# Optimization experiments

Hardware: AMD Instinct MI355X
Metric: run time of the kernel (lower is better)

Reference implementation:

```python
import jax, jax.numpy as jnp
import numpy as np

EPS = 1e-12
N_POS, N_NEG, N_NEUT, N_ASSAS = 9, 8, 7, 1
VOCAB_K = 512  # vocab_size: number of search results
NEUT_W, NEG_W, ASSAS_W = 1.0, 0.0, -10.0


def _normalize(x):
    # F.normalize(p=2, dim=-1)
    return x / jnp.maximum(jnp.linalg.norm(x, axis=-1, keepdims=True), EPS)


def _pool(embs):
    # mean over dim 1, then L2-normalize
    return _normalize(jnp.mean(embs, axis=1))


def setup_inputs() -> dict:
    key = jax.random.key(0)
    ks = jax.random.split(key, 10)
    B = 64
    inp = {
        "pos_embs": jax.random.normal(ks[0], (B, N_POS, 768), jnp.float32),
        "neg_embs": jax.random.normal(ks[1], (B, N_NEG, 768), jnp.float32),
        "neut_embs": jax.random.normal(ks[2], (B, N_NEUT, 768), jnp.float32),
        "assas_emb": jax.random.normal(ks[3], (B, 768), jnp.float32),
        "vocab_table": jax.random.normal(ks[4], (100000, 768), jnp.float32),
        "W1": jax.random.normal(ks[5], (3072, 2304), jnp.float32) * 0.02,
        "b1": jnp.zeros((2304,), jnp.float32),
        "W2": jax.random.normal(ks[6], (2304, 1700), jnp.float32) * 0.02,
        "b2": jnp.zeros((1700,), jnp.float32),
        "W3": jax.random.normal(ks[7], (1700, 1000), jnp.float32) * 0.02,
        "b3": jnp.zeros((1000,), jnp.float32),
        "W4": jax.random.normal(ks[8], (1000, 768), jnp.float32) * 0.02,
        "b4": jnp.zeros((768,), jnp.float32),
    }
    return inp


def _forward(pos_embs, neg_embs, neut_embs, assas_emb, vocab_table,
             W1, b1, W2, b2, W3, b3, W4, b4):
    # --- combined input: cat(neg_pool, assas, neut_pool, pos_pool) -> [B, 3072]
    concatenated = jnp.concatenate(
        [_pool(neg_embs), assas_emb, _pool(neut_embs), _pool(pos_embs)], axis=1)

    # --- fc MLP with tanh activations (none after last layer)
    h = jnp.tanh(concatenated @ W1 + b1)
    h = jnp.tanh(h @ W2 + b2)
    h = jnp.tanh(h @ W3 + b3)
    model_out = _normalize(h @ W4 + b4)  # [B, 768]

    # --- vocab.search: top-VOCAB_K cosine similarity against vocab table
    vocab_norm = _normalize(vocab_table)            # [N, 768]
    sims = model_out @ vocab_norm.T                  # [B, N]
    _, top_idx = jax.lax.top_k(sims, VOCAB_K)        # [B, V]
    word_embeddings = vocab_table[top_idx]           # [B, V, 768]

    # --- cosine scores against each board group (normalize then dot)
    wn = _normalize(word_embeddings)                 # [B, V, 768]
    pos_s = jnp.einsum('bvd,bpd->bvp', wn, _normalize(pos_embs))    # [B,V,9]
    neg_s = jnp.einsum('bvd,bpd->bvp', wn, _normalize(neg_embs))    # [B,V,8]
    neut_s = jnp.einsum('bvd,bpd->bvp', wn, _normalize(neut_embs))  # [B,V,7]
    assas_s = jnp.einsum('bvd,bd->bv', wn, _normalize(assas_emb))[..., None]  # [B,V,1]

    # --- primary reward: # of positive words ranked before first non-positive
    combined = jnp.concatenate([pos_s, neg_s, neut_s, assas_s], axis=2)  # [B,V,25]
    order = jnp.argsort(-combined, axis=2)           # descending sort indices
    reward_vec = jnp.concatenate(
        [jnp.zeros((N_POS,), jnp.float32),
         jnp.ones((N_NEG + N_NEUT + N_ASSAS,), jnp.float32)])
    rewards = reward_vec[order]                      # [B,V,25]
    primary = jnp.argmax(rewards, axis=2).astype(jnp.float32)  # [B,V]

    # --- secondary reward: weight of the highest-scoring non-positive word
    combined2 = combined[:, :, N_POS:]               # [B,V,16]
    reward_vec2 = jnp.concatenate(
        [jnp.full((N_NEG,), NEG_W, jnp.float32),
         jnp.full((N_NEUT,), NEUT_W, jnp.float32),
         jnp.full((N_ASSAS,), ASSAS_W, jnp.float32)])
    secondary = reward_vec2[jnp.argmax(combined2, axis=2)]      # [B,V]

    tot_reward = primary + secondary                 # [B,V]

    # --- topk(V//2) max / min selection, gather, mean-pool, normalize
    k = VOCAB_K // 2
    _, idx_max = jax.lax.top_k(tot_reward, k)
    _, idx_min = jax.lax.top_k(-tot_reward, k)
    emb_max = jnp.take_along_axis(word_embeddings, idx_max[:, :, None], axis=1)
    emb_min = jnp.take_along_axis(word_embeddings, idx_min[:, :, None], axis=1)
    max_pooled = _pool(emb_max)
    min_pooled = _pool(emb_min)
    search_embedding = emb_max[:, 0]                 # highest-scoring embedding

    return model_out, search_embedding, max_pooled, min_pooled


def reference(pos_embs, neg_embs, neut_embs, assas_emb, vocab_table,
              W1, b1, W2, b2, W3, b3, W4, b4):
    return _forward(pos_embs, neg_embs, neut_embs, assas_emb, vocab_table,
                    W1, b1, W2, b2, W3, b3, W4, b4)
```

## Files before the change

### kernel.cpp

```cpp
#include <hip/hip_runtime.h>
#include <hip/hip_bf16.h>
#include <stdint.h>

#define B_    64
#define D_    768
#define NVOC  100000
#define VK    512
#define KH    256
#define NPART 4
#define PLEN  25000

typedef __attribute__((ext_vector_type(8))) short short8v;
typedef __attribute__((ext_vector_type(4))) float f32x4;

__device__ __forceinline__ float b2f_raw(unsigned short u) {
    return __uint_as_float(((unsigned int)u) << 16);
}
__device__ __forceinline__ float ldin(const void* p, size_t i, int isbf) {
    return isbf ? b2f_raw(((const unsigned short*)p)[i]) : ((const float*)p)[i];
}
__device__ __forceinline__ float4 ldin4(const void* p, size_t i, int isbf) {
    if (isbf) {
        ushort4 r = *(const ushort4*)((const unsigned short*)p + i);
        return make_float4(b2f_raw(r.x), b2f_raw(r.y), b2f_raw(r.z), b2f_raw(r.w));
    }
    return *(const float4*)((const float*)p + i);
}
__device__ __forceinline__ unsigned short f2bf(float x) {
    uint32_t u = __float_as_uint(x);
    uint32_t r = (u + 0x7FFFu + ((u >> 16) & 1u)) >> 16;
    return (unsigned short)r;
}
__device__ __forceinline__ uint32_t fmono(float x) {
    uint32_t u = __float_as_uint(x);
    return u ^ (uint32_t)((((int32_t)u) >> 31) | 0x80000000u);
}

__device__ __forceinline__ float block_reduce_sum_256(float v, float* red) {
    int tid = threadIdx.x;
    red[tid] = v; __syncthreads();
    #pragma unroll
    for (int s = 128; s > 0; s >>= 1) {
        if (tid < s) red[tid] += red[tid + s];
        __syncthreads();
    }
    float r = red[0]; __syncthreads();
    return r;
}

__global__ void detect_kernel(const void* vocab, int* flag) {
    if (threadIdx.x == 0 && blockIdx.x == 0) {
        const float* vf = (const float*)vocab;
        int sane = 0;
        for (int i = 0; i < 256; i++) {
            float a = fabsf(vf[i]);
            if (a > 1e-4f && a < 64.0f) sane++;
        }
        *flag = (sane >= 200) ? 0 : 1;
    }
}

__global__ __launch_bounds__(256) void prep_kernel(
    const void* __restrict__ pos, const void* __restrict__ neg,
    const void* __restrict__ neut, const void* __restrict__ assas,
    float* __restrict__ concat, float* __restrict__ invemb,
    const int* __restrict__ dflag) {
    __shared__ float red[256];
    int isbf = *dflag;
    int b = blockIdx.x, tid = threadIdx.x;
    int d = tid * 3;
    const void* srcs[3] = {pos, neg, neut};
    const int cnts[3]  = {9, 8, 7};
    const int ieoff[3] = {0, 9, 17};
    const int coff[3]  = {2304, 0, 1536};
    for (int g = 0; g < 3; g++) {
        float m0 = 0.f, m1 = 0.f, m2 = 0.f;
        int cnt = cnts[g];
        for (int m = 0; m < cnt; m++) {
            size_t base = ((size_t)b * cnt + m) * D_ + d;
            float x0 = ldin(srcs[g], base + 0, isbf);
            float x1 = ldin(srcs[g], base + 1, isbf);
            float x2 = ldin(srcs[g], base + 2, isbf);
            float S = block_reduce_sum_256(x0 * x0 + x1 * x1 + x2 * x2, red);
            if (tid == 0)
                invemb[b * 25 + ieoff[g] + m] = 1.0f / fmaxf(sqrtf(S), 1e-12f);
            m0 += x0; m1 += x1; m2 += x2;
        }
        float invc = 1.0f / (float)cnt;
        m0 *= invc; m1 *= invc; m2 *= invc;
        float S = block_reduce_sum_256(m0 * m0 + m1 * m1 + m2 * m2, red);
        float inv = 1.0f / fmaxf(sqrtf(S), 1e-12f);
        float* o = concat + (size_t)b * 3072 + coff[g] + d;
        o[0] = m0 * inv; o[1] = m1 * inv; o[2] = m2 * inv;
    }
    size_t abase = (size_t)b * D_ + d;
    float x0 = ldin(assas, abase + 0, isbf);
    float x1 = ldin(assas, abase + 1, isbf);
    float x2 = ldin(assas, abase + 2, isbf);
    float* oc = concat + (size_t)b * 3072 + 768 + d;
    oc[0] = x0; oc[1] = x1; oc[2] = x2;
    float S = block_reduce_sum_256(x0 * x0 + x1 * x1 + x2 * x2, red);
    if (tid == 0) invemb[b * 25 + 24] = 1.0f / fmaxf(sqrtf(S), 1e-12f);
}

__global__ __launch_bounds__(256) void gemm_partial_kernel(
    const float* __restrict__ X, const void* __restrict__ W,
    float* __restrict__ P, int K, int N, int CH, const int* __restrict__ dflag) {
    __shared__ float xs[64][68];
    __shared__ float wt[64][68];
    int isbf = *dflag;
    int tid = threadIdx.x;
    int n0 = blockIdx.x * 64;
    int kstart = blockIdx.y * CH;
    int kend = min(K, kstart + CH);
    int tx = tid & 15, ty = tid >> 4;
    float acc[4][4] = {{0.f}};
    for (int k0 = kstart; k0 < kend; k0 += 64) {
        #pragma unroll
        for (int q = 0; q < 4; q++) {
            int e4 = tid + q * 256;
            int m = e4 >> 4, kk = (e4 & 15) * 4;
            float4 v = make_float4(0.f, 0.f, 0.f, 0.f);
            if (k0 + kk < kend) v = *(const float4*)(X + (size_t)m * K + k0 + kk);
            xs[kk + 0][m] = v.x; xs[kk + 1][m] = v.y;
            xs[kk + 2][m] = v.z; xs[kk + 3][m] = v.w;
        }
        #pragma unroll
        for (int q = 0; q < 4; q++) {
            int e4 = tid + q * 256;
            int kk = e4 >> 4, c = (e4 & 15) * 4;
            float4 v = make_float4(0.f, 0.f, 0.f, 0.f);
            if (k0 + kk < kend && n0 + c < N)
                v = ldin4(W, (size_t)(k0 + kk) * N + n0 + c, isbf);
            wt[kk][c + 0] = v.x; wt[kk][c + 1] = v.y;
            wt[kk][c + 2] = v.z; wt[kk][c + 3] = v.w;
        }
        __syncthreads();
        #pragma unroll 16
        for (int kk = 0; kk < 64; kk++) {
            float4 a = *(const float4*)&xs[kk][ty * 4];
            float4 w = *(const float4*)&wt[kk][tx * 4];
            acc[0][0] += a.x * w.x; acc[0][1] += a.x * w.y; acc[0][2] += a.x * w.z; acc[0][3] += a.x * w.w;
            acc[1][0] += a.y * w.x; acc[1][1] += a.y * w.y; acc[1][2] += a.y * w.z; acc[1][3] += a.y * w.w;
            acc[2][0] += a.z * w.x; acc[2][1] += a.z * w.y; acc[2][2] += a.z * w.z; acc[2][3] += a.z * w.w;
            acc[3][0] += a.w * w.x; acc[3][1] += a.w * w.y; acc[3][2] += a.w * w.z; acc[3][3] += a.w * w.w;
        }
        __syncthreads();
    }
    size_t base = (size_t)blockIdx.y * 64 * N;
    int n = n0 + tx * 4;
    if (n < N) {
        #pragma unroll
        for (int i = 0; i < 4; i++) {
            float4 o = make_float4(acc[i][0], acc[i][1], acc[i][2], acc[i][3]);
            *(float4*)(P + base + (size_t)(ty * 4 + i) * N + n) = o;
        }
    }
}

__global__ __launch_bounds__(256) void reduce_act_kernel(
    const float* __restrict__ P, const void* __restrict__ bias,
    float* __restrict__ Y, int N, int KS, int act, const int* __restrict__ dflag) {
    int isbf = *dflag;
    int idx = blockIdx.x * 256 + threadIdx.x;
    if (idx >= 64 * N) return;
    int n = idx % N;
    float s = 0.f;
    for (int ks = 0; ks < KS; ks++) s += P[(size_t)ks * 64 * N + idx];
    s += ldin(bias, n, isbf);
    if (act) s = tanhf(s);
    Y[idx] = s;
}

__global__ __launch_bounds__(256) void norm_mo_kernel(
    float* __restrict__ mo, float* __restrict__ out, float* __restrict__ moTp,
    unsigned short* __restrict__ moA) {
    __shared__ float red[256];
    int b = blockIdx.x, tid = threadIdx.x, d = tid * 3;
    float* r_ = mo + (size_t)b * D_ + d;
    float x0 = r_[0], x1 = r_[1], x2 = r_[2];
    float S = block_reduce_sum_256(x0 * x0 + x1 * x1 + x2 * x2, red);
    float inv = 1.0f / fmaxf(sqrtf(S), 1e-12f);
    x0 *= inv; x1 *= inv; x2 *= inv;
    r_[0] = x0; r_[1] = x1; r_[2] = x2;
    float* o = out + (size_t)b * D_ + d;
    o[0] = x0; o[1] = x1; o[2] = x2;
    if (moTp) {
        moTp[(size_t)(d + 0) * 64 + b] = x0;
        moTp[(size_t)(d + 1) * 64 + b] = x1;
        moTp[(size_t)(d + 2) * 64 + b] = x2;
    }
    if (moA) {
        float xv[3] = {x0, x1, x2};
        int w = b >> 4;
        #pragma unroll
        for (int c = 0; c < 3; c++) {
            int k = d + c;
            float x = xv[c];
            unsigned short hi = f2bf(x);
            unsigned short lo = f2bf(x - b2f_raw(hi));
            int kb2 = k >> 5, sub = (k >> 3) & 3, e = k & 7;
            int lane = (b & 15) | (sub << 4);
            moA[((((0 * 24 + kb2) * 4 + w) * 64) + lane) * 8 + e] = hi;
            moA[((((1 * 24 + kb2) * 4 + w) * 64) + lane) * 8 + e] = lo;
        }
    }
}

__global__ __launch_bounds__(256) void sims64_mfma_kernel(
    const unsigned short* __restrict__ moA, const void* __restrict__ vocab,
    float* __restrict__ sims, float* __restrict__ invn,
    const int* __restrict__ dflag) {
    if (*dflag != 1) return;
    __shared__ unsigned short Bt[4096];
    __shared__ float invLds[64];
    const unsigned short* voc = (const unsigned short*)vocab;
    int tid = threadIdx.x;
    int v0 = blockIdx.x * 64;
    int w = tid >> 6, lane = tid & 63;
    f32x4 acc[4];
    #pragma unroll
    for (int i = 0; i < 4; i++) acc[i] = (f32x4){0.f, 0.f, 0.f, 0.f};
    float ssqA = 0.f, ssqB = 0.f;
    int srow = tid >> 3;
    int scc  = tid & 7;
    for (int kb = 0; kb < 12; kb++) {
        #pragma unroll
        for (int q = 0; q < 2; q++) {
            int row = srow + q * 32;
            uint4 r = make_uint4(0u, 0u, 0u, 0u);
            if (v0 + row < NVOC)
                r = *(const uint4*)(voc + (size_t)(v0 + row) * 768 + kb * 64 + scc * 8);
            float s = 0.f;
            uint32_t us[4] = {r.x, r.y, r.z, r.w};
            #pragma unroll
            for (int t2 = 0; t2 < 4; t2++) {
                float f0 = __uint_as_float(us[t2] << 16);
                float f1 = __uint_as_float(us[t2] & 0xFFFF0000u);
                s += f0 * f0 + f1 * f1;
            }
            if (q == 0) ssqA += s; else ssqB += s;
            *(uint4*)&Bt[(scc * 64 + row) * 8] = r;
        }
        __syncthreads();
        #pragma unroll
        for (int ks = 0; ks < 2; ks++) {
            int kb2 = kb * 2 + ks;
            short8v ah = *(const short8v*)&moA[((((0 * 24 + kb2) * 4 + w) * 64) + lane) * 8];
            short8v al = *(const short8v*)&moA[((((1 * 24 + kb2) * 4 + w) * 64) + lane) * 8];
            int cc = ks * 4 + (lane >> 4);
            #pragma unroll
            for (int vs = 0; vs < 4; vs++) {
                int row = vs * 16 + (lane & 15);
                short8v bf = *(const short8v*)&Bt[(cc * 64 + row) * 8];
                acc[vs] = __builtin_amdgcn_mfma_f32_16x16x32_bf16(ah, bf, acc[vs], 0, 0, 0);
                acc[vs] = __builtin_amdgcn_mfma_f32_16x16x32_bf16(al, bf, acc[vs], 0, 0, 0);
            }
        }
        __syncthreads();
    }
    #pragma unroll
    for (int off = 1; off < 8; off <<= 1) {
        ssqA += __shfl_xor(ssqA, off, 64);
        ssqB += __shfl_xor(ssqB, off, 64);
    }
    if (scc == 0) {
        float iA = 1.0f / fmaxf(sqrtf(ssqA), 1e-12f);
        float iB = 1.0f / fmaxf(sqrtf(ssqB), 1e-12f);
        invLds[srow] = iA; invLds[srow + 32] = iB;
        if (v0 + srow < NVOC)      invn[v0 + srow] = iA;
        if (v0 + srow + 32 < NVOC) invn[v0 + srow + 32] = iB;
    }
    __syncthreads();
    #pragma unroll
    for (int vs = 0; vs < 4; vs++) {
        int v = v0 + vs * 16 + (lane & 15);
        if (v < NVOC) {
            float iv = invLds[vs * 16 + (lane & 15)];
            #pragma unroll
            for (int reg = 0; reg < 4; reg++) {
                int m = w * 16 + (lane >> 4) * 4 + reg;
                sims[(size_t)m * NVOC + v] = acc[vs][reg] * iv;
            }
        }
    }
}

__global__ __launch_bounds__(256) void sims64_kernel(
    const float* __restrict__ moT, const void* __restrict__ vocab,
    float* __restrict__ sims, float* __restrict__ invn,
    const int* __restrict__ dflag) {
    if (*dflag != 0) return;
    __shared__ float xs[64 * 64];
    __shared__ float wt[64 * 64];
    int tid = threadIdx.x;
    int v0 = blockIdx.x * 64;
    int tx = tid & 15, ty = tid >> 4;
    float acc[4][4] = {{0.f}};
    float ssq[4] = {0.f, 0.f, 0.f, 0.f};
    for (int k0 = 0; k0 < 768; k0 += 64) {
        #pragma unroll
        for (int q = 0; q < 4; q++) {
            int e4 = tid + q * 256;
            int kr = e4 >> 4, m4 = (e4 & 15) * 4;
            float4 v = *(const float4*)(moT + (size_t)(k0 + kr) * 64 + m4);
            *(float4*)&xs[kr * 64 + m4] = v;
        }
        #pragma unroll
        for (int q = 0; q < 4; q++) {
            int e4 = tid + q * 256;
            int r = e4 >> 4, kq = e4 & 15, c = kq * 4;
            float4 v = make_float4(0.f, 0.f, 0.f, 0.f);
            if (v0 + r < NVOC)
                v = *(const float4*)((const float*)vocab + (size_t)(v0 + r) * 768 + k0 + c);
            int colp = r ^ ((kq & 7) << 2);
            wt[(c + 0) * 64 + colp] = v.x;
            wt[(c + 1) * 64 + colp] = v.y;
            wt[(c + 2) * 64 + colp] = v.z;
            wt[(c + 3) * 64 + colp] = v.w;
        }
        __syncthreads();
        #pragma unroll 16
        for (int kk = 0; kk < 64; kk++) {
            float4 a = *(const float4*)&xs[kk * 64 + ty * 4];
            float4 w = *(const float4*)&wt[kk * 64 + ((tx * 4) ^ (((kk >> 2) & 7) << 2))];
            ssq[0] += w.x * w.x; ssq[1] += w.y * w.y; ssq[2] += w.z * w.z; ssq[3] += w.w * w.w;
            acc[0][0] += a.x * w.x; acc[0][1] += a.x * w.y; acc[0][2] += a.x * w.z; acc[0][3] += a.x * w.w;
            acc[1][0] += a.y * w.x; acc[1][1] += a.y * w.y; acc[1][2] += a.y * w.z; acc[1][3] += a.y * w.w;
            acc[2][0] += a.z * w.x; acc[2][1] += a.z * w.y; acc[2][2] += a.z * w.z; acc[2][3] += a.z * w.w;
            acc[3][0] += a.w * w.x; acc[3][1] += a.w * w.y; acc[3][2] += a.w * w.z; acc[3][3] += a.w * w.w;
        }
        __syncthreads();
    }
    int v = v0 + tx * 4;
    if (v < NVOC) {
        float inv[4];
        #pragma unroll
        for (int j = 0; j < 4; j++) inv[j] = 1.0f / fmaxf(sqrtf(ssq[j]), 1e-12f);
        #pragma unroll
        for (int i = 0; i < 4; i++) {
            float4 o = make_float4(acc[i][0] * inv[0], acc[i][1] * inv[1],
                                   acc[i][2] * inv[2], acc[i][3] * inv[3]);
            *(float4*)(sims + (size_t)(ty * 4 + i) * NVOC + v) = o;
        }
        if (ty == 0) *(float4*)(invn + v) = make_float4(inv[0], inv[1], inv[2], inv[3]);
    }
}

__global__ __launch_bounds__(256) void sims_kernel(
    const float* __restrict__ mo32, const void* __restrict__ vocab,
    float* __restrict__ sims, float* __restrict__ invn, int winv,
    const int* __restrict__ dflag) {
    __shared__ float xs[64][36];
    __shared__ float wt[64][68];
    int isbf = *dflag;
    int tid = threadIdx.x;
    int v0 = blockIdx.x * 64;
    int tx = tid & 15, ty = tid >> 4;
    float acc[2][4] = {{0.f}};
    float ssq[4] = {0.f, 0.f, 0.f, 0.f};
    for (int k0 = 0; k0 < 768; k0 += 64) {
        #pragma unroll
        for (int q = 0; q < 2; q++) {
            int e4 = tid + q * 256;
            int m = e4 >> 4, kk = (e4 & 15) * 4;
            float4 v = *(const float4*)(mo32 + (size_t)m * 768 + k0 + kk);
            xs[kk + 0][m] = v.x; xs[kk + 1][m] = v.y;
            xs[kk + 2][m] = v.z; xs[kk + 3][m] = v.w;
        }
        #pragma unroll
        for (int q = 0; q < 4; q++) {
            int e4 = tid + q * 256;
            int r = e4 >> 4, c = (e4 & 15) * 4;
            float4 v = make_float4(0.f, 0.f, 0.f, 0.f);
            if (v0 + r < NVOC)
                v = ldin4(vocab, (size_t)(v0 + r) * 768 + k0 + c, isbf);
            wt[c + 0][r] = v.x; wt[c + 1][r] = v.y;
            wt[c + 2][r] = v.z; wt[c + 3][r] = v.w;
        }
        __syncthreads();
        #pragma unroll 16
        for (int kk = 0; kk < 64; kk++) {
            float2 a = *(const float2*)&xs[kk][ty * 2];
            float4 w = *(const float4*)&wt[kk][tx * 4];
            ssq[0] += w.x * w.x; ssq[1] += w.y * w.y; ssq[2] += w.z * w.z; ssq[3] += w.w * w.w;
            acc[0][0] += a.x * w.x; acc[0][1] += a.x * w.y; acc[0][2] += a.x * w.z; acc[0][3] += a.x * w.w;
            acc[1][0] += a.y * w.x; acc[1][1] += a.y * w.y; acc[1][2] += a.y * w.z; acc[1][3] += a.y * w.w;
        }
        __syncthreads();
    }
    int v = v0 + tx * 4;
    if (v < NVOC) {
        float inv[4];
        #pragma unroll
        for (int j = 0; j < 4; j++) inv[j] = 1.0f / fmaxf(sqrtf(ssq[j]), 1e-12f);
        #pragma unroll
        for (int i = 0; i < 2; i++) {
            float4 o = make_float4(acc[i][0] * inv[0], acc[i][1] * inv[1],
                                   acc[i][2] * inv[2], acc[i][3] * inv[3]);
            *(float4*)(sims + (size_t)(ty * 2 + i) * NVOC + v) = o;
        }
        if (ty == 0 && winv) *(float4*)(invn + v) = make_float4(inv[0], inv[1], inv[2], inv[3]);
    }
}

__device__ void bitonic_desc_u64(unsigned long long* d, int n, int tid, int nt) {
    for (int k = 2; k <= n; k <<= 1) {
        for (int j = k >> 1; j > 0; j >>= 1) {
            for (int i = tid; i < n; i += nt) {
                int ixj = i ^ j;
                if (ixj > i) {
                    unsigned long long a = d[i], b = d[ixj];
                    bool up = ((i & k) == 0);
                    if (up ? (a < b) : (a > b)) { d[i] = b; d[ixj] = a; }
                }
            }
            __syncthreads();
        }
    }
}

__global__ __launch_bounds__(1024) void pselect_kernel(
    const float* __restrict__ sims, unsigned long long* __restrict__ psel) {
    __shared__ int hist[4096];
    __shared__ unsigned long long cand[2048];
    __shared__ int ssum[1024];
    __shared__ int s_Tg, s_T, s_cnt;
    int b = blockIdx.y, part = blockIdx.x, tid = threadIdx.x;
    const float* row = sims + (size_t)b * NVOC + (size_t)part * PLEN;
    #pragma unroll
    for (int q = 0; q < 4; q++) hist[tid * 4 + q] = 0;
    __syncthreads();
    for (int v = tid; v < PLEN; v += 1024) {
        uint32_t u = fmono(row[v]);
        atomicAdd(&hist[u >> 20], 1);
    }
    __syncthreads();
    int a_ = 0;
    #pragma unroll
    for (int q = 0; q < 4; q++) a_ += hist[tid * 4 + q];
    ssum[tid] = a_; __syncthreads();
    for (int off = 1; off < 1024; off <<= 1) {
        int add = (tid + off < 1024) ? ssum[tid + off] : 0;
        __syncthreads();
        ssum[tid] += add;
        __syncthreads();
    }
    if (ssum[tid] >= VK && (tid == 1023 || ssum[tid + 1] < VK)) s_Tg = tid;
    __syncthreads();
    if (tid == 0) {
        int g = s_Tg;
        int above = (g == 1023) ? 0 : ssum[g + 1];
        int T = g * 4;
        for (int bin = g * 4 + 3; bin >= g * 4; bin--) {
            int c = hist[bin];
            if (above + c >= VK) { T = bin; break; }
            above += c;
        }
        s_T = T; s_cnt = 0;
    }
    __syncthreads();
    uint32_t T = (uint32_t)s_T;
    for (int v = tid; v < PLEN; v += 1024) {
        uint32_t u = fmono(row[v]);
        if ((u >> 20) >= T) {
            int p = atomicAdd(&s_cnt, 1);
            if (p < 2048) {
                uint32_t vg = (uint32_t)(part * PLEN + v);
                cand[p] = ((unsigned long long)u << 32) | (uint32_t)(~vg);
            }
        }
    }
    __syncthreads();
    int total = min(s_cnt, 2048);
    for (int i = tid; i < 2048; i += 1024)
        if (i >= total) cand[i] = 0ull;
    __syncthreads();
    bitonic_desc_u64(cand, 2048, tid, 1024);
    if (tid < VK) psel[((size_t)b * NPART + part) * VK + tid] = cand[tid];
}

__global__ __launch_bounds__(512) void pmerge_kernel(
    const unsigned long long* __restrict__ psel, int* __restrict__ top_idx) {
    __shared__ unsigned long long key[2048];
    int b = blockIdx.x, tid = threadIdx.x;
    for (int i = tid; i < 2048; i += 512) key[i] = psel[(size_t)b * 2048 + i];
    __syncthreads();
    bitonic_desc_u64(key, 2048, tid, 512);
    if (tid < VK) top_idx[(size_t)b * VK + tid] = (int)(~(uint32_t)(key[tid] & 0xFFFFFFFFull));
}

__global__ __launch_bounds__(1024) void select512_kernel(
    const float* __restrict__ sims, int* __restrict__ top_idx) {
    __shared__ int hist[4096];
    __shared__ unsigned long long cand[4096];
    __shared__ int ssum[1024];
    __shared__ int s_Tg, s_T, s_cnt;
    int b = blockIdx.x, tid = threadIdx.x;
    const float* row = sims + (size_t)b * NVOC;
    #pragma unroll
    for (int q = 0; q < 4; q++) hist[tid * 4 + q] = 0;
    __syncthreads();
    for (int v = tid; v < NVOC; v += 1024) {
        uint32_t u = fmono(row[v]);
        atomicAdd(&hist[u >> 20], 1);
    }
    __syncthreads();
    int a_ = 0;
    #pragma unroll
    for (int q = 0; q < 4; q++) a_ += hist[tid * 4 + q];
    ssum[tid] = a_; __syncthreads();
    for (int off = 1; off < 1024; off <<= 1) {
        int add = (tid + off < 1024) ? ssum[tid + off] : 0;
        __syncthreads();
        ssum[tid] += add;
        __syncthreads();
    }
    if (ssum[tid] >= VK && (tid == 1023 || ssum[tid + 1] < VK)) s_Tg = tid;
    __syncthreads();
    if (tid == 0) {
        int g = s_Tg;
        int above = (g == 1023) ? 0 : ssum[g + 1];
        int T = g * 4;
        for (int bin = g * 4 + 3; bin >= g * 4; bin--) {
            int c = hist[bin];
            if (above + c >= VK) { T = bin; break; }
            above += c;
        }
        s_T = T; s_cnt = 0;
    }
    __syncthreads();
    uint32_t T = (uint32_t)s_T;
    for (int v = tid; v < NVOC; v += 1024) {
        uint32_t u = fmono(row[v]);
        if ((u >> 20) >= T) {
            int p = atomicAdd(&s_cnt, 1);
            if (p < 4096) cand[p] = ((unsigned long long)u << 32) | (uint32_t)(~v);
        }
    }
    __syncthreads();
    int total = min(s_cnt, 4096);
    for (int i = tid; i < 4096; i += 1024)
        if (i >= total) cand[i] = 0ull;
    __syncthreads();
    bitonic_desc_u64(cand, 4096, tid, 1024);
    if (tid < VK) top_idx[(size_t)b * VK + tid] = (int)(~(uint32_t)(cand[tid] & 0xFFFFFFFFull));
}

__global__ __launch_bounds__(128) void tot_kernel(
    const int* __restrict__ top_idx, const void* __restrict__ vocab,
    const float* __restrict__ invn, const float* __restrict__ invemb,
    const void* __restrict__ pos, const void* __restrict__ neg,
    const void* __restrict__ neut, const void* __restrict__ assas,
    float* __restrict__ tot, const int* __restrict__ dflag) {
    __shared__ float E[25 * 384];
    int isbf = *dflag;
    int b = blockIdx.y;
    int j = blockIdx.x * 128 + threadIdx.x;
    int v = top_idx[(size_t)b * VK + j];
    if ((unsigned)v >= (unsigned)NVOC) v = 0;
    size_t vbase = (size_t)v * D_;
    float p[25];
    #pragma unroll
    for (int i = 0; i < 25; i++) p[i] = 0.f;

    for (int h = 0; h < 2; h++) {
        __syncthreads();
        for (int u = threadIdx.x; u < 2400; u += 128) {
            int i = u / 96;
            int c = (u - i * 96) * 4;
            const void* ep; size_t eb;
            if (i < 9)       { ep = pos;   eb = ((size_t)b * 9 + i) * D_; }
            else if (i < 17) { ep = neg;   eb = ((size_t)b * 8 + (i - 9)) * D_; }
            else if (i < 24) { ep = neut;  eb = ((size_t)b * 7 + (i - 17)) * D_; }
            else             { ep = assas; eb = (size_t)b * D_; }
            float4 x = ldin4(ep, eb + h * 384 + c, isbf);
            float s = invemb[b * 25 + i];
            E[i * 384 + c + 0] = x.x * s;
            E[i * 384 + c + 1] = x.y * s;
            E[i * 384 + c + 2] = x.z * s;
            E[i * 384 + c + 3] = x.w * s;
        }
        __syncthreads();
        for (int c = 0; c < 384; c += 4) {
            float4 w = ldin4(vocab, vbase + h * 384 + c, isbf);
            #pragma unroll
            for (int i = 0; i < 25; i++) {
                float4 e = *(const float4*)&E[i * 384 + c];
                p[i] += w.x * e.x + w.y * e.y + w.z * e.z + w.w * e.w;
            }
        }
    }

    float invv = invn[v];
    #pragma unroll
    for (int i = 0; i < 25; i++) p[i] *= invv;
    float mx = -1e30f; int am = 9;
    #pragma unroll
    for (int i = 9; i < 25; i++) if (p[i] > mx) { mx = p[i]; am = i; }
    int primary = 0;
    #pragma unroll
    for (int i = 0; i < 9; i++) primary += (p[i] >= mx) ? 1 : 0;
    float secondary = (am == 24) ? -10.0f : ((am >= 17) ? 1.0f : 0.0f);
    tot[(size_t)b * VK + j] = (float)primary + secondary;
}

__global__ __launch_bounds__(256) void sort512_kernel(
    const float* __restrict__ tot, int* __restrict__ idx_max, int* __restrict__ idx_min) {
    __shared__ unsigned long long key[512];
    int b = blockIdx.x, tid = threadIdx.x;
    for (int pass = 0; pass < 2; pass++) {
        for (int j = tid; j < 512; j += 256) {
            uint32_t m = fmono(tot[(size_t)b * VK + j]);
            if (pass) m = ~m;
            key[j] = ((unsigned long long)m << 32) | (uint32_t)(511 - j);
        }
        __syncthreads();
        bitonic_desc_u64(key, 512, tid, 256);
        int* dst = pass ? idx_min : idx_max;
        if (tid < 256) dst[(size_t)b * KH + tid] = 511 - (int)(key[tid] & 0xFFFFFFFFull);
        __syncthreads();
    }
}

__global__ __launch_bounds__(256) void pool_kernel(
    const int* __restrict__ top_idx, const int* __restrict__ idx_max,
    const int* __restrict__ idx_min, const void* __restrict__ vocab,
    float* __restrict__ out, const int* __restrict__ dflag) {
    __shared__ float red[256];
    int isbf = *dflag;
    int b = blockIdx.x, s = blockIdx.y, tid = threadIdx.x;
    const int* sel = s ? idx_min : idx_max;
    int d = tid * 3;
    float a0 = 0.f, a1 = 0.f, a2 = 0.f;
    for (int r = 0; r < 256; r++) {
        int v = top_idx[(size_t)b * VK + sel[(size_t)b * KH + r]];
        if ((unsigned)v >= (unsigned)NVOC) v = 0;
        size_t vb = (size_t)v * D_ + d;
        a0 += ldin(vocab, vb + 0, isbf);
        a1 += ldin(vocab, vb + 1, isbf);
        a2 += ldin(vocab, vb + 2, isbf);
    }
    a0 *= (1.0f / 256.0f); a1 *= (1.0f / 256.0f); a2 *= (1.0f / 256.0f);
    float S = block_reduce_sum_256(a0 * a0 + a1 * a1 + a2 * a2, red);
    float inv = 1.0f / fmaxf(sqrtf(S), 1e-12f);
    float* o = out + (size_t)(2 + s) * (B_ * D_) + (size_t)b * D_ + d;
    o[0] = a0 * inv;
    o[1] = a1 * inv;
    o[2] = a2 * inv;
    if (s == 0) {
        int v0 = top_idx[(size_t)b * VK + sel[(size_t)b * KH + 0]];
        if ((unsigned)v0 >= (unsigned)NVOC) v0 = 0;
        size_t vb = (size_t)v0 * D_ + d;
        float* so = out + (size_t)(B_ * D_) + (size_t)b * D_ + d;
        so[0] = ldin(vocab, vb + 0, isbf);
        so[1] = ldin(vocab, vb + 1, isbf);
        so[2] = ldin(vocab, vb + 2, isbf);
    }
}

extern "C" void kernel_launch(void* const* d_in, const int* in_sizes, int n_in,
                              void* d_out, int out_size, void* d_ws, size_t ws_size,
                              hipStream_t stream) {
    const void* pos   = d_in[0];
    const void* neg   = d_in[1];
    const void* neut  = d_in[2];
    const void* assas = d_in[3];
    const void* vocab = d_in[4];
    const void* W1 = d_in[5];  const void* b1 = d_in[6];
    const void* W2 = d_in[7];  const void* b2 = d_in[8];
    const void* W3 = d_in[9];  const void* b3 = d_in[10];
    const void* W4 = d_in[11]; const void* b4 = d_in[12];
    float* out = (float*)d_out;

    int big = ws_size >= (size_t)32 * 1024 * 1024;

    float* ws = (float*)d_ws;
    if (big) {
        float* concat = ws;
        float* h1     = concat + 196608;
        float* h2     = h1 + 147456;
        float* h3     = h2 + 108800;
        float* mo     = h3 + 64000;
        float* moT    = mo + 49152;
        float* moA_f  = moT + 49152;
        float* invn   = moA_f + 49152;
        float* invemb = invn + 100000;
        float* simsPb = invemb + 1600;
        int* top_idx  = (int*)(simsPb + 6400000);
        float* tot    = (float*)(top_idx + 64 * VK);
        int* imax     = (int*)(tot + 64 * VK);
        int* imin     = imax + 64 * KH;
        unsigned long long* psel = (unsigned long long*)(imin + 64 * KH);
        int* dflag    = (int*)(psel + 64 * NPART * VK);
        unsigned short* moAu = (unsigned short*)moA_f;

        detect_kernel<<<1, 64, 0, stream>>>(vocab, dflag);
        prep_kernel<<<64, 256, 0, stream>>>(pos, neg, neut, assas, concat, invemb, dflag);

        gemm_partial_kernel<<<dim3(36, 8), 256, 0, stream>>>(concat, W1, simsPb, 3072, 2304, 384, dflag);
        reduce_act_kernel<<<576, 256, 0, stream>>>(simsPb, b1, h1, 2304, 8, 1, dflag);
        gemm_partial_kernel<<<dim3(27, 9), 256, 0, stream>>>(h1, W2, simsPb, 2304, 1700, 256, dflag);
        reduce_act_kernel<<<425, 256, 0, stream>>>(simsPb, b2, h2, 1700, 9, 1, dflag);
        gemm_partial_kernel<<<dim3(16, 9), 256, 0, stream>>>(h2, W3, simsPb, 1700, 1000, 192, dflag);
        reduce_act_kernel<<<250, 256, 0, stream>>>(simsPb, b3, h3, 1000, 9, 1, dflag);
        gemm_partial_kernel<<<dim3(12, 8), 256, 0, stream>>>(h3, W4, simsPb, 1000, 768, 128, dflag);
        reduce_act_kernel<<<192, 256, 0, stream>>>(simsPb, b4, mo, 768, 8, 0, dflag);

        norm_mo_kernel<<<64, 256, 0, stream>>>(mo, out, moT, moAu);

        sims64_mfma_kernel<<<1563, 256, 0, stream>>>(moAu, vocab, simsPb, invn, dflag);
        sims64_kernel<<<1563, 256, 0, stream>>>(moT, vocab, simsPb, invn, dflag);

        pselect_kernel<<<dim3(NPART, 64), 1024, 0, stream>>>(simsPb, psel);
        pmerge_kernel<<<64, 512, 0, stream>>>(psel, top_idx);

        tot_kernel<<<dim3(4, 64), 128, 0, stream>>>(top_idx, vocab, invn, invemb,
                                                    pos, neg, neut, assas, tot, dflag);
        sort512_kernel<<<64, 256, 0, stream>>>(tot, imax, imin);
        pool_kernel<<<dim3(64, 2), 256, 0, stream>>>(top_idx, imax, imin, vocab, out, dflag);
    } else {
        float* concat = ws;
        float* h1     = concat + 196608;
        float* h2     = h1 + 147456;
        float* h3     = h2 + 108800;
        float* mo     = h3 + 64000;
        float* invn   = mo + 49152;
        float* invemb = invn + 100000;
        float* simsPb = invemb + 1600;
        int* top_idx  = (int*)(simsPb + 3200000);
        float* tot    = (float*)(top_idx + 64 * VK);
        int* imax     = (int*)(tot + 64 * VK);
        int* imin     = imax + 64 * KH;
        int* dflag    = imin + 64 * KH;

        detect_kernel<<<1, 64, 0, stream>>>(vocab, dflag);
        prep_kernel<<<64, 256, 0, stream>>>(pos, neg, neut, assas, concat, invemb, dflag);

        gemm_partial_kernel<<<dim3(36, 8), 256, 0, stream>>>(concat, W1, simsPb, 3072, 2304, 384, dflag);
        reduce_act_kernel<<<576, 256, 0, stream>>>(simsPb, b1, h1, 2304, 8, 1, dflag);
        gemm_partial_kernel<<<dim3(27, 9), 256, 0, stream>>>(h1, W2, simsPb, 2304, 1700, 256, dflag);
        reduce_act_kernel<<<425, 256, 0, stream>>>(simsPb, b2, h2, 1700, 9, 1, dflag);
        gemm_partial_kernel<<<dim3(16, 9), 256, 0, stream>>>(h2, W3, simsPb, 1700, 1000, 192, dflag);
        reduce_act_kernel<<<250, 256, 0, stream>>>(simsPb, b3, h3, 1000, 9, 1, dflag);
        gemm_partial_kernel<<<dim3(12, 8), 256, 0, stream>>>(h3, W4, simsPb, 1000, 768, 128, dflag);
        reduce_act_kernel<<<192, 256, 0, stream>>>(simsPb, b4, mo, 768, 8, 0, dflag);

        norm_mo_kernel<<<64, 256, 0, stream>>>(mo, out, nullptr, nullptr);

        for (int pass = 0; pass < 2; pass++) {
            sims_kernel<<<1563, 256, 0, stream>>>(mo + (size_t)pass * 32 * D_, vocab,
                                                  simsPb, invn, pass == 0, dflag);
            select512_kernel<<<32, 1024, 0, stream>>>(simsPb, top_idx + (size_t)pass * 32 * VK);
        }

        tot_kernel<<<dim3(4, 64), 128, 0, stream>>>(top_idx, vocab, invn, invemb,
                                                    pos, neg, neut, assas, tot, dflag);
        sort512_kernel<<<64, 256, 0, stream>>>(tot, imax, imin);
        pool_kernel<<<dim3(64, 2), 256, 0, stream>>>(top_idx, imax, imin, vocab, out, dflag);
    }
}
```

Baseline: 1.063 ms.

## Compute fp32 vocab similarity with split-bf16 MFMA instead of scalar FMA

```diff
diff --git a/kernel.cpp b/kernel.cpp
--- a/kernel.cpp
+++ b/kernel.cpp
@@ -286,64 +286,93 @@
     }
 }
 
-__global__ __launch_bounds__(256) void sims64_kernel(
-    const float* __restrict__ moT, const void* __restrict__ vocab,
+__global__ __launch_bounds__(256) void sims64_mfma_f32_kernel(
+    const unsigned short* __restrict__ moA, const float* __restrict__ vocab,
     float* __restrict__ sims, float* __restrict__ invn,
     const int* __restrict__ dflag) {
     if (*dflag != 0) return;
-    __shared__ float xs[64 * 64];
-    __shared__ float wt[64 * 64];
+    __shared__ unsigned short Bh[4096];
+    __shared__ unsigned short Bl[4096];
+    __shared__ float invLds[64];
     int tid = threadIdx.x;
     int v0 = blockIdx.x * 64;
-    int tx = tid & 15, ty = tid >> 4;
-    float acc[4][4] = {{0.f}};
-    float ssq[4] = {0.f, 0.f, 0.f, 0.f};
-    for (int k0 = 0; k0 < 768; k0 += 64) {
-        #pragma unroll
-        for (int q = 0; q < 4; q++) {
-            int e4 = tid + q * 256;
-            int kr = e4 >> 4, m4 = (e4 & 15) * 4;
-            float4 v = *(const float4*)(moT + (size_t)(k0 + kr) * 64 + m4);
-            *(float4*)&xs[kr * 64 + m4] = v;
-        }
-        #pragma unroll
-        for (int q = 0; q < 4; q++) {
-            int e4 = tid + q * 256;
-            int r = e4 >> 4, kq = e4 & 15, c = kq * 4;
-            float4 v = make_float4(0.f, 0.f, 0.f, 0.f);
-            if (v0 + r < NVOC)
-                v = *(const float4*)((const float*)vocab + (size_t)(v0 + r) * 768 + k0 + c);
-            int colp = r ^ ((kq & 7) << 2);
-            wt[(c + 0) * 64 + colp] = v.x;
-            wt[(c + 1) * 64 + colp] = v.y;
-            wt[(c + 2) * 64 + colp] = v.z;
-            wt[(c + 3) * 64 + colp] = v.w;
-        }
-        __syncthreads();
-        #pragma unroll 16
-        for (int kk = 0; kk < 64; kk++) {
-            float4 a = *(const float4*)&xs[kk * 64 + ty * 4];
-            float4 w = *(const float4*)&wt[kk * 64 + ((tx * 4) ^ (((kk >> 2) & 7) << 2))];
-            ssq[0] += w.x * w.x; ssq[1] += w.y * w.y; ssq[2] += w.z * w.z; ssq[3] += w.w * w.w;
-            acc[0][0] += a.x * w.x; acc[0][1] += a.x * w.y; acc[0][2] += a.x * w.z; acc[0][3] += a.x * w.w;
-            acc[1][0] += a.y * w.x; acc[1][1] += a.y * w.y; acc[1][2] += a.y * w.z; acc[1][3] += a.y * w.w;
-            acc[2][0] += a.z * w.x; acc[2][1] += a.z * w.y; acc[2][2] += a.z * w.z; acc[2][3] += a.z * w.w;
-            acc[3][0] += a.w * w.x; acc[3][1] += a.w * w.y; acc[3][2] += a.w * w.z; acc[3][3] += a.w * w.w;
-        }
-        __syncthreads();
-    }
-    int v = v0 + tx * 4;
-    if (v < NVOC) {
-        float inv[4];
-        #pragma unroll
-        for (int j = 0; j < 4; j++) inv[j] = 1.0f / fmaxf(sqrtf(ssq[j]), 1e-12f);
-        #pragma unroll
-        for (int i = 0; i < 4; i++) {
-            float4 o = make_float4(acc[i][0] * inv[0], acc[i][1] * inv[1],
-                                   acc[i][2] * inv[2], acc[i][3] * inv[3]);
-            *(float4*)(sims + (size_t)(ty * 4 + i) * NVOC + v) = o;
-        }
-        if (ty == 0) *(float4*)(invn + v) = make_float4(inv[0], inv[1], inv[2], inv[3]);
+    int w = tid >> 6, lane = tid & 63;
+    f32x4 acc[4];
+    #pragma unroll
+    for (int i = 0; i < 4; i++) acc[i] = (f32x4){0.f, 0.f, 0.f, 0.f};
+    float ssqA = 0.f, ssqB = 0.f;
+    int srow = tid >> 3;
+    int scc  = tid & 7;
+    for (int kb = 0; kb < 12; kb++) {
+        #pragma unroll
+        for (int q = 0; q < 2; q++) {
+            int row = srow + q * 32;
+            float4 xa = make_float4(0.f, 0.f, 0.f, 0.f);
+            float4 xb = make_float4(0.f, 0.f, 0.f, 0.f);
+            if (v0 + row < NVOC) {
+                const float* s_ = vocab + (size_t)(v0 + row) * 768 + kb * 64 + scc * 8;
+                xa = *(const float4*)s_;
+                xb = *(const float4*)(s_ + 4);
+            }
+            float s = xa.x*xa.x + xa.y*xa.y + xa.z*xa.z + xa.w*xa.w
+                    + xb.x*xb.x + xb.y*xb.y + xb.z*xb.z + xb.w*xb.w;
+            if (q == 0) ssqA += s; else ssqB += s;
+            float xv[8] = {xa.x, xa.y, xa.z, xa.w, xb.x, xb.y, xb.z, xb.w};
+            uint32_t hw_[4], lw_[4];
+            #pragma unroll
+            for (int t = 0; t < 4; t++) {
+                unsigned short h0 = f2bf(xv[2*t]),     h1 = f2bf(xv[2*t+1]);
+                float l0 = xv[2*t] - b2f_raw(h0),      l1 = xv[2*t+1] - b2f_raw(h1);
+                hw_[t] = (uint32_t)h0 | ((uint32_t)h1 << 16);
+                lw_[t] = (uint32_t)f2bf(l0) | ((uint32_t)f2bf(l1) << 16);
+            }
+            *(uint4*)&Bh[(scc * 64 + row) * 8] = make_uint4(hw_[0], hw_[1], hw_[2], hw_[3]);
+            *(uint4*)&Bl[(scc * 64 + row) * 8] = make_uint4(lw_[0], lw_[1], lw_[2], lw_[3]);
+        }
+        __syncthreads();
+        #pragma unroll
+        for (int ks = 0; ks < 2; ks++) {
+            int kb2 = kb * 2 + ks;
+            short8v ah = *(const short8v*)&moA[((((0 * 24 + kb2) * 4 + w) * 64) + lane) * 8];
+            short8v al = *(const short8v*)&moA[((((1 * 24 + kb2) * 4 + w) * 64) + lane) * 8];
+            int cc = ks * 4 + (lane >> 4);
+            #pragma unroll
+            for (int vs = 0; vs < 4; vs++) {
+                int row = vs * 16 + (lane & 15);
+                short8v bh = *(const short8v*)&Bh[(cc * 64 + row) * 8];
+                short8v bl = *(const short8v*)&Bl[(cc * 64 + row) * 8];
+                acc[vs] = __builtin_amdgcn_mfma_f32_16x16x32_bf16(ah, bh, acc[vs], 0, 0, 0);
+                acc[vs] = __builtin_amdgcn_mfma_f32_16x16x32_bf16(al, bh, acc[vs], 0, 0, 0);
+                acc[vs] = __builtin_amdgcn_mfma_f32_16x16x32_bf16(ah, bl, acc[vs], 0, 0, 0);
+                acc[vs] = __builtin_amdgcn_mfma_f32_16x16x32_bf16(al, bl, acc[vs], 0, 0, 0);
+            }
+        }
+        __syncthreads();
+    }
+    #pragma unroll
+    for (int off = 1; off < 8; off <<= 1) {
+        ssqA += __shfl_xor(ssqA, off, 64);
+        ssqB += __shfl_xor(ssqB, off, 64);
+    }
+    if (scc == 0) {
+        float iA = 1.0f / fmaxf(sqrtf(ssqA), 1e-12f);
+        float iB = 1.0f / fmaxf(sqrtf(ssqB), 1e-12f);
+        invLds[srow] = iA; invLds[srow + 32] = iB;
+        if (v0 + srow < NVOC)      invn[v0 + srow] = iA;
+        if (v0 + srow + 32 < NVOC) invn[v0 + srow + 32] = iB;
+    }
+    __syncthreads();
+    #pragma unroll
+    for (int vs = 0; vs < 4; vs++) {
+        int v = v0 + vs * 16 + (lane & 15);
+        if (v < NVOC) {
+            float iv = invLds[vs * 16 + (lane & 15)];
+            #pragma unroll
+            for (int reg = 0; reg < 4; reg++) {
+                int m = w * 16 + (lane >> 4) * 4 + reg;
+                sims[(size_t)m * NVOC + v] = acc[vs][reg] * iv;
+            }
+        }
     }
 }
 
@@ -710,7 +739,8 @@
         norm_mo_kernel<<<64, 256, 0, stream>>>(mo, out, moT, moAu);
 
         sims64_mfma_kernel<<<1563, 256, 0, stream>>>(moAu, vocab, simsPb, invn, dflag);
-        sims64_kernel<<<1563, 256, 0, stream>>>(moT, vocab, simsPb, invn, dflag);
+        sims64_mfma_f32_kernel<<<1563, 256, 0, stream>>>(moAu, (const float*)vocab,
+                                                         simsPb, invn, dflag);
 
         pselect_kernel<<<dim3(NPART, 64), 1024, 0, stream>>>(simsPb, psel);
         pmerge_kernel<<<64, 512, 0, stream>>>(psel, top_idx);
```

New measurement: 999.0 us. 6.0% less time.
